# Performance work log

Measured on AMD Instinct MI355X. Metric: run time of the kernel, lower is better.

Reference implementation:

```python
import jax, jax.numpy as jnp
import numpy as np

IN_CH = 128
OUT_CH = 128
N_NODES = 50000
N_EDGES = 800000
BN_EPS = 1e-5


def setup_inputs() -> dict:
    key = jax.random.key(0)
    k_x, k_e, k_wl, k_bl, k_wr = jax.random.split(key, 5)
    x = jax.random.normal(k_x, (N_NODES, IN_CH), dtype=jnp.float32)
    edge_index = jax.random.randint(k_e, (2, N_EDGES), 0, N_NODES, dtype=jnp.int64)
    s = 1.0 / np.sqrt(IN_CH)
    W_l = jax.random.uniform(k_wl, (OUT_CH, IN_CH), jnp.float32, -s, s)  # lin_l: aggregated neighbors
    b_l = jax.random.uniform(k_bl, (OUT_CH,), jnp.float32, -s, s)
    W_r = jax.random.uniform(k_wr, (OUT_CH, IN_CH), jnp.float32, -s, s)  # lin_r: root/self
    gamma = jnp.ones((OUT_CH,), jnp.float32)
    beta = jnp.zeros((OUT_CH,), jnp.float32)
    return {"x": x, "edge_index": edge_index, "W_l": W_l, "b_l": b_l,
            "W_r": W_r, "gamma": gamma, "beta": beta}


def reference(x, edge_index, W_l, b_l, W_r, gamma, beta):
    n = x.shape[0]
    src, dst = edge_index[0], edge_index[1]
    # gather source features and mean-aggregate at destination nodes
    msgs = x[src]                                              # [E, C_in]
    agg = jax.ops.segment_sum(msgs, dst, num_segments=n)      # [N, C_in]
    deg = jax.ops.segment_sum(jnp.ones((edge_index.shape[1],), x.dtype), dst, num_segments=n)
    mean_agg = agg / jnp.maximum(deg, 1.0)[:, None]
    # SAGEConv: lin_l(aggregated) + lin_r(self)
    h = mean_agg @ W_l.T + b_l + x @ W_r.T                     # [N, C_out]
    # BatchNorm1d (training-mode batch statistics, biased variance)
    mu = h.mean(axis=0)
    var = ((h - mu) ** 2).mean(axis=0)
    h = (h - mu) * jax.lax.rsqrt(var + BN_EPS) * gamma + beta
    return jax.nn.relu(h)
```

## Files before the change

### kernel.cpp

```cpp
#include <hip/hip_runtime.h>

#define CH 128
#define BN_EPS 1e-5f

typedef unsigned int uint32;
typedef unsigned short ushort16;
using f32x4  = __attribute__((ext_vector_type(4))) float;
using bf16x8 = __attribute__((ext_vector_type(8))) short;

__device__ __forceinline__ ushort16 f2b(float f) {
    uint32 u = __float_as_uint(f);
    return (ushort16)((u + 0x7FFFu + ((u >> 16) & 1u)) >> 16);
}
__device__ __forceinline__ uint32 pk2(float a, float b) {
    return (uint32)f2b(a) | ((uint32)f2b(b) << 16);
}

__global__ __launch_bounds__(256) void sage_prep(
    const float* __restrict__ x, const void* __restrict__ ei,
    const float* __restrict__ Wl, const float* __restrict__ Wr,
    int* __restrict__ head, int2* __restrict__ pair,
    uint32* __restrict__ xb4, uint2* __restrict__ xq8,
    ushort16* __restrict__ wct, float* __restrict__ bn,
    int nEdges, int total8)
{
    const int* pi = (const int*)ei;
    int lane = threadIdx.x & 63;
    int probe = pi[lane * 2 + 1];
    bool is64 = (__ballot(probe != 0) == 0ULL);

    int idx = blockIdx.x * 256 + threadIdx.x;
    int e0 = idx * 2, e1 = e0 + 1;
    if (e0 < nEdges) {
        bool has1 = (e1 < nEdges);
        int s0, d0, s1 = 0, d1 = 0;
        if (is64) {
            const long long* p = (const long long*)ei;
            long long a0 = p[e0];
            long long a1 = has1 ? p[e1] : 0;
            long long b0 = p[nEdges + e0];
            long long b1 = has1 ? p[nEdges + e1] : 0;
            s0 = (int)a0; s1 = (int)a1; d0 = (int)b0; d1 = (int)b1;
        } else {
            s0 = pi[e0]; s1 = has1 ? pi[e1] : 0;
            d0 = pi[nEdges + e0]; d1 = has1 ? pi[nEdges + e1] : 0;
        }
        int old0 = atomicExch(&head[d0], e0);
        int old1 = has1 ? atomicExch(&head[d1], e1) : 0;
        if (has1) {
            int4 pk = make_int4(old0, s0, old1, s1);
            *(int4*)(pair + e0) = pk;
        } else {
            pair[e0] = make_int2(old0, s0);
        }
    }

    int i0 = idx * 2, i1 = i0 + 1;
    if (i0 < total8) {
        const float4* x4 = (const float4*)x;
        float4 a = x4[2 * i0], b = x4[2 * i0 + 1];
        bool has1 = (i1 < total8);
        float4 c = has1 ? x4[2 * i1] : make_float4(0, 0, 0, 0);
        float4 d = has1 ? x4[2 * i1 + 1] : make_float4(0, 0, 0, 0);

        uint4 o0 = make_uint4(pk2(a.x, a.y), pk2(a.z, a.w), pk2(b.x, b.y), pk2(b.z, b.w));
        ((uint4*)xb4)[i0] = o0;
        if (has1) {
            uint4 o1 = make_uint4(pk2(c.x, c.y), pk2(c.z, c.w), pk2(d.x, d.y), pk2(d.z, d.w));
            ((uint4*)xb4)[i1] = o1;
        }

        int qa = __builtin_amdgcn_cvt_pk_fp8_f32(a.x, a.y, 0, false);
        qa = __builtin_amdgcn_cvt_pk_fp8_f32(a.z, a.w, qa, true);
        int qb = __builtin_amdgcn_cvt_pk_fp8_f32(b.x, b.y, 0, false);
        qb = __builtin_amdgcn_cvt_pk_fp8_f32(b.z, b.w, qb, true);
        if (has1) {
            int qc = __builtin_amdgcn_cvt_pk_fp8_f32(c.x, c.y, 0, false);
            qc = __builtin_amdgcn_cvt_pk_fp8_f32(c.z, c.w, qc, true);
            int qd = __builtin_amdgcn_cvt_pk_fp8_f32(d.x, d.y, 0, false);
            qd = __builtin_amdgcn_cvt_pk_fp8_f32(d.z, d.w, qd, true);
            *(uint4*)(xq8 + i0) = make_uint4((uint32)qa, (uint32)qb, (uint32)qc, (uint32)qd);
        } else {
            xq8[i0] = make_uint2((uint32)qa, (uint32)qb);
        }
    }

    if (blockIdx.x < 128) {
        int widx = blockIdx.x * 256 + threadIdx.x;
        int co = widx >> 8, k = widx & 255;
        float v = (k < 128) ? Wr[co * 128 + k] : Wl[co * 128 + (k - 128)];
        wct[widx] = f2b(v);
    }
    if (blockIdx.x == 0) bn[threadIdx.x] = 0.f;
    if (blockIdx.x == 1 && threadIdx.x < 32)
        ((uint32*)(xq8))[(size_t)total8 * 2 + threadIdx.x] = 0;
}

__global__ __launch_bounds__(256) void sage_aggregate(
    const char* __restrict__ xq, const int* __restrict__ head,
    const int2* __restrict__ pair, uint32* __restrict__ mean_b, int nNodes)
{
    int wid = blockIdx.x * 4 + (threadIdx.x >> 6);
    int nbase = wid * 8;
    if (nbase >= nNodes) return;
    int lane = threadIdx.x & 63;
    int chain = lane >> 3;
    int sub = lane & 7;

    const int ZROW = nNodes;

    int cur = -1;
    if (lane < 8) {
        int n = nbase + lane;
        cur = (n < nNodes) ? head[n] : -1;
    }
    int cnt = 0;
    float acc[16];
    #pragma unroll
    for (int i = 0; i < 16; ++i) acc[i] = 0.f;

    while (__ballot(cur >= 0) != 0ULL) {
        int2 pr = make_int2(-1, ZROW);
        if (cur >= 0) pr = pair[cur];
        int s = __shfl(pr.y, chain);
        uint4 u = *(const uint4*)(xq + ((size_t)s << 7) + sub * 16);
        #pragma unroll
        for (int w = 0; w < 4; ++w) {
            uint32 uw = (&u.x)[w];
            acc[w * 4 + 0] += __builtin_amdgcn_cvt_f32_fp8(uw, 0);
            acc[w * 4 + 1] += __builtin_amdgcn_cvt_f32_fp8(uw, 1);
            acc[w * 4 + 2] += __builtin_amdgcn_cvt_f32_fp8(uw, 2);
            acc[w * 4 + 3] += __builtin_amdgcn_cvt_f32_fp8(uw, 3);
        }
        if (cur >= 0) { ++cnt; cur = pr.x; }
    }

    int cn = __shfl(cnt, chain);
    float inv = 1.0f / fmaxf((float)cn, 1.0f);
    int n = nbase + chain;
    if (n < nNodes) {
        uint4 o0 = make_uint4(pk2(acc[0] * inv, acc[1] * inv),
                              pk2(acc[2] * inv, acc[3] * inv),
                              pk2(acc[4] * inv, acc[5] * inv),
                              pk2(acc[6] * inv, acc[7] * inv));
        uint4 o1 = make_uint4(pk2(acc[8] * inv, acc[9] * inv),
                              pk2(acc[10] * inv, acc[11] * inv),
                              pk2(acc[12] * inv, acc[13] * inv),
                              pk2(acc[14] * inv, acc[15] * inv));
        char* base = (char*)mean_b + (size_t)n * 256 + sub * 32;
        *(uint4*)base = o0;
        *(uint4*)(base + 16) = o1;
    }
}

__global__ __launch_bounds__(256) void sage_gemm(
    const ushort16* __restrict__ xb, const ushort16* __restrict__ mean_b,
    const ushort16* __restrict__ wct, const float* __restrict__ bl,
    float* __restrict__ h, float* __restrict__ bn, int nNodes)
{
    __shared__ ushort16 wsh[8 * 8 * 64 * 8];
    __shared__ float redS[4][CH];
    __shared__ float redQ[4][CH];

    int tid = threadIdx.x;
    int wave = tid >> 6, lane = tid & 63;
    int col = lane & 15, kg = lane >> 4;

    #pragma unroll
    for (int it = 0; it < 16; ++it) {
        int pidx = wave * 16 + it;
        int cb = pidx >> 3, ks = pidx & 7;
        bf16x8 v = *(const bf16x8*)(wct + (size_t)(cb * 16 + col) * 256 + ks * 32 + kg * 8);
        *(bf16x8*)(wsh + ((size_t)pidx * 64 + lane) * 8) = v;
    }

    int rowBase = blockIdx.x * 64 + wave * 16;
    int arow = min(rowBase + col, nNodes - 1);
    const ushort16* xrow = xb + (size_t)arow * CH;
    const ushort16* mrow = mean_b + (size_t)arow * CH;

    bf16x8 afrag[8];
    #pragma unroll
    for (int t = 0; t < 4; ++t)
        afrag[t] = *(const bf16x8*)(xrow + t * 32 + kg * 8);
    #pragma unroll
    for (int t = 0; t < 4; ++t)
        afrag[4 + t] = *(const bf16x8*)(mrow + t * 32 + kg * 8);

    __syncthreads();

    f32x4 acc[8];
    #pragma unroll
    for (int cb = 0; cb < 8; ++cb) acc[cb] = (f32x4){0.f, 0.f, 0.f, 0.f};

    #pragma unroll
    for (int kstep = 0; kstep < 8; ++kstep) {
        bf16x8 a = afrag[kstep];
        #pragma unroll
        for (int cb = 0; cb < 8; ++cb) {
            bf16x8 b = *(const bf16x8*)(wsh + ((size_t)(cb * 8 + kstep) * 64 + lane) * 8);
            acc[cb] = __builtin_amdgcn_mfma_f32_16x16x32_bf16(a, b, acc[cb], 0, 0, 0);
        }
    }

    #pragma unroll
    for (int cb = 0; cb < 8; ++cb) {
        int co = cb * 16 + col;
        float blv = bl[co];
        float s = 0.f, ss = 0.f;
        #pragma unroll
        for (int j = 0; j < 4; ++j) {
            int r = rowBase + kg * 4 + j;
            float v = acc[cb][j] + blv;
            if (r < nNodes) {
                h[(size_t)r * CH + co] = v;
                s += v;
                ss += v * v;
            }
        }
        s  += __shfl_xor(s, 16);  s  += __shfl_xor(s, 32);
        ss += __shfl_xor(ss, 16); ss += __shfl_xor(ss, 32);
        if (kg == 0) { redS[wave][co] = s; redQ[wave][co] = ss; }
    }
    __syncthreads();
    if (tid < CH) {
        atomicAdd(&bn[tid], redS[0][tid] + redS[1][tid] + redS[2][tid] + redS[3][tid]);
    } else {
        int c = tid - CH;
        atomicAdd(&bn[CH + c], redQ[0][c] + redQ[1][c] + redQ[2][c] + redQ[3][c]);
    }
}

__global__ __launch_bounds__(256) void sage_apply(
    float* __restrict__ h, const float* __restrict__ bn,
    const float* __restrict__ gamma, const float* __restrict__ beta,
    int total4, int nNodes)
{
    __shared__ float sc_sh[CH], sh_sh[CH];
    int tid = threadIdx.x;
    if (tid < CH) {
        float invN = 1.0f / (float)nNodes;
        float mu = bn[tid] * invN;
        float var = fmaxf(bn[CH + tid] * invN - mu * mu, 0.f);
        float sc = gamma[tid] * rsqrtf(var + BN_EPS);
        sc_sh[tid] = sc;
        sh_sh[tid] = beta[tid] - mu * sc;
    }
    __syncthreads();
    int i = blockIdx.x * 256 + tid;
    if (i >= total4) return;
    float4 v = reinterpret_cast<float4*>(h)[i];
    int c = (i * 4) & 127;
    float4 sc = *reinterpret_cast<const float4*>(&sc_sh[c]);
    float4 sh = *reinterpret_cast<const float4*>(&sh_sh[c]);
    v.x = fmaxf(fmaf(v.x, sc.x, sh.x), 0.f);
    v.y = fmaxf(fmaf(v.y, sc.y, sh.y), 0.f);
    v.z = fmaxf(fmaf(v.z, sc.z, sh.z), 0.f);
    v.w = fmaxf(fmaf(v.w, sc.w, sh.w), 0.f);
    reinterpret_cast<float4*>(h)[i] = v;
}

extern "C" void kernel_launch(void* const* d_in, const int* in_sizes, int n_in,
                              void* d_out, int out_size, void* d_ws, size_t ws_size,
                              hipStream_t stream)
{
    const float* x     = (const float*)d_in[0];
    const void*  ei    = d_in[1];
    const float* Wl    = (const float*)d_in[2];
    const float* bl    = (const float*)d_in[3];
    const float* Wr    = (const float*)d_in[4];
    const float* gamma = (const float*)d_in[5];
    const float* beta  = (const float*)d_in[6];

    int nNodes = in_sizes[0] / CH;
    int nEdges = in_sizes[1] / 2;
    int nBlkM  = (nNodes + 63) / 64;

    char* p = (char*)d_ws;
    auto take = [&](size_t bytes) {
        char* r = p;
        p += (bytes + 255) & ~(size_t)255;
        return r;
    };
    ushort16* xb      = (ushort16*)take((size_t)nNodes * CH * 2);
    char*     xq      = (char*)take((size_t)nNodes * CH + 128);
    ushort16* mean_b  = (ushort16*)take((size_t)nNodes * CH * 2);
    ushort16* wct     = (ushort16*)take((size_t)CH * 256 * 2);
    int*      head    = (int*)take((size_t)nNodes * 4);
    float*    bn      = (float*)take(256 * 4);
    int2*     pair    = (int2*)take((size_t)nEdges * 8);

    float* h = (float*)d_out;

    hipMemsetAsync(head, 0xFF, (size_t)nNodes * 4, stream);

    int total8 = nNodes * CH / 8;
    int ePairs = (nEdges + 1) / 2;
    int cPairs = (total8 + 1) / 2;
    int pBlocks = (max(ePairs, cPairs) + 255) / 256;
    sage_prep<<<pBlocks, 256, 0, stream>>>(
        x, ei, Wl, Wr, head, pair, (uint32*)xb, (uint2*)xq, wct, bn,
        nEdges, total8);

    int aBlocks = (nNodes + 31) / 32;
    sage_aggregate<<<aBlocks, 256, 0, stream>>>(
        xq, head, pair, (uint32*)mean_b, nNodes);

    sage_gemm<<<nBlkM, 256, 0, stream>>>(
        xb, mean_b, wct, bl, h, bn, nNodes);

    int total4 = nNodes * CH / 4;
    sage_apply<<<(total4 + 255) / 256, 256, 0, stream>>>(
        h, bn, gamma, beta, total4, nNodes);
}
```

Measured before the change: 125.3 us.

## Store pre-norm activations in bf16 and simplify prep and aggregation conversions

The GEMM now writes pre-BatchNorm activations as bf16 to a workspace buffer instead of fp32 to the output. The apply kernel reads these bf16 values and writes fp32 output, which cuts the intermediate write/read traffic for h. Prep now handles one edge and one 8-channel chunk per thread instead of two. Aggregation uses packed fp8-to-f32x2 conversions. The trade-off is bf16 rounding error in the normalized output, an extra workspace buffer, and more prep threads.

```diff
diff --git a/kernel.cpp b/kernel.cpp
--- a/kernel.cpp
+++ b/kernel.cpp
@@ -5,6 +5,7 @@
 
 typedef unsigned int uint32;
 typedef unsigned short ushort16;
+using f32x2  = __attribute__((ext_vector_type(2))) float;
 using f32x4  = __attribute__((ext_vector_type(4))) float;
 using bf16x8 = __attribute__((ext_vector_type(8))) short;
 
@@ -15,6 +16,8 @@
 __device__ __forceinline__ uint32 pk2(float a, float b) {
     return (uint32)f2b(a) | ((uint32)f2b(b) << 16);
 }
+__device__ __forceinline__ float blo(uint32 u) { return __uint_as_float(u << 16); }
+__device__ __forceinline__ float bhi(uint32 u) { return __uint_as_float(u & 0xFFFF0000u); }
 
 __global__ __launch_bounds__(256) void sage_prep(
     const float* __restrict__ x, const void* __restrict__ ei,
@@ -30,59 +33,37 @@
     bool is64 = (__ballot(probe != 0) == 0ULL);
 
     int idx = blockIdx.x * 256 + threadIdx.x;
-    int e0 = idx * 2, e1 = e0 + 1;
-    if (e0 < nEdges) {
-        bool has1 = (e1 < nEdges);
-        int s0, d0, s1 = 0, d1 = 0;
+
+    const float4* x4 = (const float4*)x;
+    float4 a = make_float4(0, 0, 0, 0), b = make_float4(0, 0, 0, 0);
+    bool hasC = (idx < total8);
+    if (hasC) { a = x4[2 * idx]; b = x4[2 * idx + 1]; }
+
+    if (idx < nEdges) {
+        int s, d;
         if (is64) {
             const long long* p = (const long long*)ei;
-            long long a0 = p[e0];
-            long long a1 = has1 ? p[e1] : 0;
-            long long b0 = p[nEdges + e0];
-            long long b1 = has1 ? p[nEdges + e1] : 0;
-            s0 = (int)a0; s1 = (int)a1; d0 = (int)b0; d1 = (int)b1;
+            s = (int)p[idx];
+            d = (int)p[nEdges + idx];
         } else {
-            s0 = pi[e0]; s1 = has1 ? pi[e1] : 0;
-            d0 = pi[nEdges + e0]; d1 = has1 ? pi[nEdges + e1] : 0;
-        }
-        int old0 = atomicExch(&head[d0], e0);
-        int old1 = has1 ? atomicExch(&head[d1], e1) : 0;
-        if (has1) {
-            int4 pk = make_int4(old0, s0, old1, s1);
-            *(int4*)(pair + e0) = pk;
-        } else {
-            pair[e0] = make_int2(old0, s0);
-        }
-    }
-
-    int i0 = idx * 2, i1 = i0 + 1;
-    if (i0 < total8) {
-        const float4* x4 = (const float4*)x;
-        float4 a = x4[2 * i0], b = x4[2 * i0 + 1];
-        bool has1 = (i1 < total8);
-        float4 c = has1 ? x4[2 * i1] : make_float4(0, 0, 0, 0);
-        float4 d = has1 ? x4[2 * i1 + 1] : make_float4(0, 0, 0, 0);
-
-        uint4 o0 = make_uint4(pk2(a.x, a.y), pk2(a.z, a.w), pk2(b.x, b.y), pk2(b.z, b.w));
-        ((uint4*)xb4)[i0] = o0;
-        if (has1) {
-            uint4 o1 = make_uint4(pk2(c.x, c.y), pk2(c.z, c.w), pk2(d.x, d.y), pk2(d.z, d.w));
-            ((uint4*)xb4)[i1] = o1;
-        }
+            s = pi[idx];
+            d = pi[nEdges + idx];
+        }
+        int old = atomicExch(&head[d], idx);
+        pair[idx] = make_int2(old, s);
+    }
+
+    if (hasC) {
+        uint4 o;
+        o.x = pk2(a.x, a.y); o.y = pk2(a.z, a.w);
+        o.z = pk2(b.x, b.y); o.w = pk2(b.z, b.w);
+        ((uint4*)xb4)[idx] = o;
 
         int qa = __builtin_amdgcn_cvt_pk_fp8_f32(a.x, a.y, 0, false);
         qa = __builtin_amdgcn_cvt_pk_fp8_f32(a.z, a.w, qa, true);
         int qb = __builtin_amdgcn_cvt_pk_fp8_f32(b.x, b.y, 0, false);
         qb = __builtin_amdgcn_cvt_pk_fp8_f32(b.z, b.w, qb, true);
-        if (has1) {
-            int qc = __builtin_amdgcn_cvt_pk_fp8_f32(c.x, c.y, 0, false);
-            qc = __builtin_amdgcn_cvt_pk_fp8_f32(c.z, c.w, qc, true);
-            int qd = __builtin_amdgcn_cvt_pk_fp8_f32(d.x, d.y, 0, false);
-            qd = __builtin_amdgcn_cvt_pk_fp8_f32(d.z, d.w, qd, true);
-            *(uint4*)(xq8 + i0) = make_uint4((uint32)qa, (uint32)qb, (uint32)qc, (uint32)qd);
-        } else {
-            xq8[i0] = make_uint2((uint32)qa, (uint32)qb);
-        }
+        xq8[idx] = make_uint2((uint32)qa, (uint32)qb);
     }
 
     if (blockIdx.x < 128) {
@@ -115,9 +96,9 @@
         cur = (n < nNodes) ? head[n] : -1;
     }
     int cnt = 0;
-    float acc[16];
-    #pragma unroll
-    for (int i = 0; i < 16; ++i) acc[i] = 0.f;
+    f32x2 acc2[8];
+    #pragma unroll
+    for (int i = 0; i < 8; ++i) acc2[i] = (f32x2){0.f, 0.f};
 
     while (__ballot(cur >= 0) != 0ULL) {
         int2 pr = make_int2(-1, ZROW);
@@ -127,10 +108,8 @@
         #pragma unroll
         for (int w = 0; w < 4; ++w) {
             uint32 uw = (&u.x)[w];
-            acc[w * 4 + 0] += __builtin_amdgcn_cvt_f32_fp8(uw, 0);
-            acc[w * 4 + 1] += __builtin_amdgcn_cvt_f32_fp8(uw, 1);
-            acc[w * 4 + 2] += __builtin_amdgcn_cvt_f32_fp8(uw, 2);
-            acc[w * 4 + 3] += __builtin_amdgcn_cvt_f32_fp8(uw, 3);
+            acc2[w * 2 + 0] += __builtin_amdgcn_cvt_pk_f32_fp8((int)uw, false);
+            acc2[w * 2 + 1] += __builtin_amdgcn_cvt_pk_f32_fp8((int)uw, true);
         }
         if (cur >= 0) { ++cnt; cur = pr.x; }
     }
@@ -139,14 +118,14 @@
     float inv = 1.0f / fmaxf((float)cn, 1.0f);
     int n = nbase + chain;
     if (n < nNodes) {
-        uint4 o0 = make_uint4(pk2(acc[0] * inv, acc[1] * inv),
-                              pk2(acc[2] * inv, acc[3] * inv),
-                              pk2(acc[4] * inv, acc[5] * inv),
-                              pk2(acc[6] * inv, acc[7] * inv));
-        uint4 o1 = make_uint4(pk2(acc[8] * inv, acc[9] * inv),
-                              pk2(acc[10] * inv, acc[11] * inv),
-                              pk2(acc[12] * inv, acc[13] * inv),
-                              pk2(acc[14] * inv, acc[15] * inv));
+        uint4 o0 = make_uint4(pk2(acc2[0][0] * inv, acc2[0][1] * inv),
+                              pk2(acc2[1][0] * inv, acc2[1][1] * inv),
+                              pk2(acc2[2][0] * inv, acc2[2][1] * inv),
+                              pk2(acc2[3][0] * inv, acc2[3][1] * inv));
+        uint4 o1 = make_uint4(pk2(acc2[4][0] * inv, acc2[4][1] * inv),
+                              pk2(acc2[5][0] * inv, acc2[5][1] * inv),
+                              pk2(acc2[6][0] * inv, acc2[6][1] * inv),
+                              pk2(acc2[7][0] * inv, acc2[7][1] * inv));
         char* base = (char*)mean_b + (size_t)n * 256 + sub * 32;
         *(uint4*)base = o0;
         *(uint4*)(base + 16) = o1;
@@ -156,7 +135,7 @@
 __global__ __launch_bounds__(256) void sage_gemm(
     const ushort16* __restrict__ xb, const ushort16* __restrict__ mean_b,
     const ushort16* __restrict__ wct, const float* __restrict__ bl,
-    float* __restrict__ h, float* __restrict__ bn, int nNodes)
+    ushort16* __restrict__ hb, float* __restrict__ bn, int nNodes)
 {
     __shared__ ushort16 wsh[8 * 8 * 64 * 8];
     __shared__ float redS[4][CH];
@@ -213,7 +192,7 @@
             int r = rowBase + kg * 4 + j;
             float v = acc[cb][j] + blv;
             if (r < nNodes) {
-                h[(size_t)r * CH + co] = v;
+                hb[(size_t)r * CH + co] = f2b(v);
                 s += v;
                 ss += v * v;
             }
@@ -232,9 +211,9 @@
 }
 
 __global__ __launch_bounds__(256) void sage_apply(
-    float* __restrict__ h, const float* __restrict__ bn,
-    const float* __restrict__ gamma, const float* __restrict__ beta,
-    int total4, int nNodes)
+    const ushort16* __restrict__ hb, float* __restrict__ out,
+    const float* __restrict__ bn, const float* __restrict__ gamma,
+    const float* __restrict__ beta, int total8, int nNodes)
 {
     __shared__ float sc_sh[CH], sh_sh[CH];
     int tid = threadIdx.x;
@@ -248,16 +227,21 @@
     }
     __syncthreads();
     int i = blockIdx.x * 256 + tid;
-    if (i >= total4) return;
-    float4 v = reinterpret_cast<float4*>(h)[i];
-    int c = (i * 4) & 127;
-    float4 sc = *reinterpret_cast<const float4*>(&sc_sh[c]);
-    float4 sh = *reinterpret_cast<const float4*>(&sh_sh[c]);
-    v.x = fmaxf(fmaf(v.x, sc.x, sh.x), 0.f);
-    v.y = fmaxf(fmaf(v.y, sc.y, sh.y), 0.f);
-    v.z = fmaxf(fmaf(v.z, sc.z, sh.z), 0.f);
-    v.w = fmaxf(fmaf(v.w, sc.w, sh.w), 0.f);
-    reinterpret_cast<float4*>(h)[i] = v;
+    if (i >= total8) return;
+    uint4 u = *(const uint4*)(hb + (size_t)i * 8);
+    int c = (i * 8) & 127;
+    float4 o0, o1;
+    o0.x = fmaxf(fmaf(blo(u.x), sc_sh[c + 0], sh_sh[c + 0]), 0.f);
+    o0.y = fmaxf(fmaf(bhi(u.x), sc_sh[c + 1], sh_sh[c + 1]), 0.f);
+    o0.z = fmaxf(fmaf(blo(u.y), sc_sh[c + 2], sh_sh[c + 2]), 0.f);
+    o0.w = fmaxf(fmaf(bhi(u.y), sc_sh[c + 3], sh_sh[c + 3]), 0.f);
+    o1.x = fmaxf(fmaf(blo(u.z), sc_sh[c + 4], sh_sh[c + 4]), 0.f);
+    o1.y = fmaxf(fmaf(bhi(u.z), sc_sh[c + 5], sh_sh[c + 5]), 0.f);
+    o1.z = fmaxf(fmaf(blo(u.w), sc_sh[c + 6], sh_sh[c + 6]), 0.f);
+    o1.w = fmaxf(fmaf(bhi(u.w), sc_sh[c + 7], sh_sh[c + 7]), 0.f);
+    float4* dst = (float4*)(out + (size_t)i * 8);
+    dst[0] = o0;
+    dst[1] = o1;
 }
 
 extern "C" void kernel_launch(void* const* d_in, const int* in_sizes, int n_in,
@@ -285,19 +269,19 @@
     ushort16* xb      = (ushort16*)take((size_t)nNodes * CH * 2);
     char*     xq      = (char*)take((size_t)nNodes * CH + 128);
     ushort16* mean_b  = (ushort16*)take((size_t)nNodes * CH * 2);
+    ushort16* hb      = (ushort16*)take((size_t)nNodes * CH * 2);
     ushort16* wct     = (ushort16*)take((size_t)CH * 256 * 2);
     int*      head    = (int*)take((size_t)nNodes * 4);
     float*    bn      = (float*)take(256 * 4);
     int2*     pair    = (int2*)take((size_t)nEdges * 8);
 
-    float* h = (float*)d_out;
+    float* out = (float*)d_out;
 
     hipMemsetAsync(head, 0xFF, (size_t)nNodes * 4, stream);
 
     int total8 = nNodes * CH / 8;
-    int ePairs = (nEdges + 1) / 2;
-    int cPairs = (total8 + 1) / 2;
-    int pBlocks = (max(ePairs, cPairs) + 255) / 256;
+    int eBlocks = (nEdges + 255) / 256;
+    int pBlocks = max(eBlocks, (total8 + 255) / 256);
     sage_prep<<<pBlocks, 256, 0, stream>>>(
         x, ei, Wl, Wr, head, pair, (uint32*)xb, (uint2*)xq, wct, bn,
         nEdges, total8);
@@ -307,9 +291,8 @@
         xq, head, pair, (uint32*)mean_b, nNodes);
 
     sage_gemm<<<nBlkM, 256, 0, stream>>>(
-        xb, mean_b, wct, bl, h, bn, nNodes);
-
-    int total4 = nNodes * CH / 4;
-    sage_apply<<<(total4 + 255) / 256, 256, 0, stream>>>(
-        h, bn, gamma, beta, total4, nNodes);
-}
+        xb, mean_b, wct, bl, hb, bn, nNodes);
+
+    sage_apply<<<(total8 + 255) / 256, 256, 0, stream>>>(
+        hb, out, bn, gamma, beta, total8, nNodes);
+}
```

Result: no change. 124.6 us (-0.6%).
